# Kernel tuning notes

Hardware: AMD Instinct MI355X
Metric: run time of the kernel (lower is better)

## Reference

```python
import jax, jax.numpy as jnp
from jax import lax
import numpy as np

B, Q, C = 128, 200, 92  # batch, num_queries, num_classes (0 = no-object)


def hungarian(cost):
    """Exact Hungarian assignment (augmenting-path / JV potentials, e-maxx form).
    cost: [n, n]. Returns col_of_row: [n] int32, the column matched to each row.
    Uses 1-based columns/rows internally; index 0 is the sentinel."""
    n = cost.shape[0]
    INF = jnp.asarray(1e9, cost.dtype)

    def solve_row(i, carry):
        u, v, p = carry
        p = p.at[0].set(jnp.int32(i))
        minv = jnp.full(n + 1, INF, cost.dtype)
        way = jnp.zeros(n + 1, jnp.int32)
        used = jnp.zeros(n + 1, bool)
        state = (u, v, p, minv, way, used, jnp.int32(0))

        def cond(s):
            _u, _v, _p, _minv, _way, _used, j0 = s
            return _p[j0] != 0

        def body(s):
            u, v, p, minv, way, used, j0 = s
            used = used.at[j0].set(True)
            i0 = p[j0]
            cur = cost[i0 - 1, :] - u[i0] - v[1:]          # reduced costs of row i0
            cur = jnp.where(used[1:], INF, cur)
            upd = cur < minv[1:]
            minv = minv.at[1:].set(jnp.where(upd, cur, minv[1:]))
            way = way.at[1:].set(jnp.where(upd, j0, way[1:]))
            masked = jnp.where(used[1:], INF, minv[1:])
            j1 = jnp.argmin(masked).astype(jnp.int32) + 1
            delta = masked[j1 - 1]
            zero = jnp.asarray(0, cost.dtype)
            u = u.at[p].add(jnp.where(used, delta, zero))  # u[p[j]] += delta for used j (rows distinct)
            v = jnp.where(used, v - delta, v)
            minv = jnp.where(used, minv, minv - delta)
            return (u, v, p, minv, way, used, j1)

        u, v, p, minv, way, used, j0 = lax.while_loop(cond, body, state)

        def aug_body(s):  # flip matching along the alternating path
            p, j0 = s
            j1 = way[j0]
            return p.at[j0].set(p[j1]), j1

        p, _ = lax.while_loop(lambda s: s[1] != 0, aug_body, (p, j0))
        return (u, v, p)

    u0 = jnp.zeros(n + 1, cost.dtype)
    v0 = jnp.zeros(n + 1, cost.dtype)
    p0 = jnp.zeros(n + 1, jnp.int32)
    _, _, p = lax.fori_loop(1, n + 1, solve_row, (u0, v0, p0))
    # p[j] = row matched to column j (1-based); invert to col per row (0-based)
    col_of_row = jnp.zeros(n, jnp.int32).at[p[1:] - 1].set(jnp.arange(n, dtype=jnp.int32))
    return col_of_row


def cost_matrix(pred_cat, pred_bbox, tar_cat, tar_bbox):
    b, q, c = pred_cat.shape
    log_probs = jax.nn.log_softmax(pred_cat, axis=-1)                  # [B,Qp,C]
    idx = jnp.broadcast_to(tar_cat[:, None, :], (b, q, q))             # [B,Qp,Qt]
    ce = -jnp.take_along_axis(log_probs, idx, axis=2)                  # CE(pred_i, tgt_j)
    d = pred_bbox[:, :, None, :] - tar_bbox[:, None, :, :]             # [B,Qp,Qt,4]
    ad = jnp.abs(d)
    sl1 = jnp.where(ad < 1.0, 0.5 * d * d, ad - 0.5).sum(-1)           # SmoothL1 (beta=1)
    mask = (tar_cat != 0).astype(sl1.dtype)[:, None, :]                # bbox loss only for real objects
    return ce + sl1 * mask                                             # [B,Qp,Qt]


def setup_inputs() -> dict:
    key = jax.random.key(0)
    k1, k2, k3, k4 = jax.random.split(key, 4)
    pred_cat = jax.random.normal(k1, (B, Q, C), dtype=jnp.float32)
    pred_bbox = jax.random.uniform(k2, (B, Q, 4), dtype=jnp.float32)
    tar_cat = jax.random.randint(k3, (B, Q), 0, C, dtype=jnp.int32)
    tar_bbox = jax.random.uniform(k4, (B, Q, 4), dtype=jnp.float32)
    return {"pred_cat": pred_cat, "pred_bbox": pred_bbox, "tar_cat": tar_cat, "tar_bbox": tar_bbox}


def reference(pred_cat, pred_bbox, tar_cat, tar_bbox):
    cost = cost_matrix(pred_cat, pred_bbox, tar_cat, tar_bbox)         # [B,Q,Q]
    col = jax.vmap(hungarian)(lax.stop_gradient(cost))                 # assignment on detached cost
    out = jnp.take_along_axis(cost, col[:, :, None], axis=2)[..., 0]   # [B,Q] per-query matched loss
    return out
```

## Files before the change

kernel.cpp:

```cpp
#include <hip/hip_runtime.h>
#include <math.h>

#define BB 128
#define QQ 200
#define CC 92
#define CMPAD (QQ * QQ + 64)

__device__ __forceinline__ int rdlane_i(int x, int l) { return __builtin_amdgcn_readlane(x, l); }
__device__ __forceinline__ float rdlane_f(float x, int l) {
    return __uint_as_float((unsigned)__builtin_amdgcn_readlane((int)__float_as_uint(x), l));
}

__device__ __forceinline__ float wave_fmin_bcast(float x) {
    float y;
#define DPPSTEP(ctrl) \
    y = __uint_as_float((unsigned)__builtin_amdgcn_update_dpp( \
            (int)__float_as_uint(x), (int)__float_as_uint(x), ctrl, 0xf, 0xf, false)); \
    x = fminf(x, y);
    DPPSTEP(0x111) DPPSTEP(0x112) DPPSTEP(0x114) DPPSTEP(0x118)
    DPPSTEP(0x142) DPPSTEP(0x143)
#undef DPPSTEP
    return rdlane_f(x, 63);
}

__global__ __launch_bounds__(256) void hungarian_fused(const float* __restrict__ pc,
                                                       const float* __restrict__ pb,
                                                       const int*   __restrict__ tc,
                                                       const float* __restrict__ tb,
                                                       float* __restrict__ out) {
    const int b = blockIdx.x;
    const int tid = threadIdx.x;
    const int w = tid >> 6;
    const int t = tid & 63;

    __shared__ __align__(16) float cm[CMPAD];
    __shared__ float lse_s[QQ];

    const float INF = 1e9f;
    const int nval = (t < 8) ? 4 : 3;

    int   cls[4];
    float tbx[4][4];
#pragma unroll
    for (int k = 0; k < 4; ++k) {
        if (k < nval) {
            int jj = t + 64 * k;
            cls[k] = tc[b * QQ + jj];
            const float4 v4 = *reinterpret_cast<const float4*>(tb + ((size_t)(b * QQ + jj)) * 4);
            tbx[k][0] = v4.x; tbx[k][1] = v4.y; tbx[k][2] = v4.z; tbx[k][3] = v4.w;
        } else {
            cls[k] = 0;
            tbx[k][0] = tbx[k][1] = tbx[k][2] = tbx[k][3] = 0.f;
        }
    }

    if (tid < QQ) {
        const float* row = pc + ((size_t)(b * QQ + tid)) * CC;
        float m = -INFINITY;
        for (int c = 0; c < CC; ++c) m = fmaxf(m, row[c]);
        float s = 0.f;
        for (int c = 0; c < CC; ++c) s += expf(row[c] - m);
        lse_s[tid] = m + logf(s);
    }
    __syncthreads();

    for (int i = w; i < QQ; i += 4) {
        const float4 pb4 = *reinterpret_cast<const float4*>(pb + ((size_t)(b * QQ + i)) * 4);
        const float pbb[4] = {pb4.x, pb4.y, pb4.z, pb4.w};
        const float lsei = lse_s[i];
        const float* pcrow = pc + ((size_t)(b * QQ + i)) * CC;
#pragma unroll
        for (int k = 0; k < 4; ++k) {
            if (k < nval) {
                float ce = lsei - pcrow[cls[k]];
                float sl1 = 0.f;
#pragma unroll
                for (int d = 0; d < 4; ++d) {
                    float df = pbb[d] - tbx[k][d];
                    float ad = fabsf(df);
                    sl1 += (ad < 1.f) ? 0.5f * df * df : (ad - 0.5f);
                }
                float mask = (cls[k] != 0) ? 1.f : 0.f;
                cm[i * QQ + t + 64 * k] = ce + sl1 * mask;
            }
        }
    }
    __syncthreads();

    if (tid >= 64) return;

    float v[4]     = {0.f, 0.f, 0.f, 0.f};
    int   pslot[4] = {0, 0, 0, 0};
    unsigned pp    = 0u;
    float uslot[4] = {0.f, 0.f, 0.f, 0.f};
    float minv[4];
    int   waysl[4];
    int   usedm;
    float usent;

    for (int i = 1; i <= QQ; ++i) {
        minv[0] = minv[1] = minv[2] = minv[3] = INF;
        waysl[0] = waysl[1] = waysl[2] = waysl[3] = 0;
        usedm = 0;
        usent = 0.f;
        int j0 = 0;
        float u0 = 0.f;
        const float* crow = cm + (i - 1) * QQ;
        float c0 = crow[t];
        float c1 = crow[64 + t];
        float c2 = crow[128 + t];
        float c3 = crow[192 + t];

        for (;;) {
            if (j0 > 0) {
                int s = (j0 - 1) >> 6;
                if (((j0 - 1) & 63) == t) usedm |= 1 << s;
            }

            float kv0, kv1, kv2, kv3;
            {
                float cur;
                cur = c0 - u0 - v[0];
                if (!(usedm & 1) && cur < minv[0]) { minv[0] = cur; waysl[0] = j0; }
                kv0 = (usedm & 1) ? INF : minv[0];
                cur = c1 - u0 - v[1];
                if (!(usedm & 2) && cur < minv[1]) { minv[1] = cur; waysl[1] = j0; }
                kv1 = (usedm & 2) ? INF : minv[1];
                cur = c2 - u0 - v[2];
                if (!(usedm & 4) && cur < minv[2]) { minv[2] = cur; waysl[2] = j0; }
                kv2 = (usedm & 4) ? INF : minv[2];
                cur = c3 - u0 - v[3];
                if (!(usedm & 8) && t < 8 && cur < minv[3]) { minv[3] = cur; waysl[3] = j0; }
                kv3 = ((usedm & 8) || t >= 8) ? INF : minv[3];
            }

            float gmin = wave_fmin_bcast(fminf(fminf(kv0, kv1), fminf(kv2, kv3)));
            float delta = gmin;

            unsigned long long m0 = __ballot(kv0 == gmin);
            unsigned long long m1 = __ballot(kv1 == gmin);
            unsigned long long m2 = __ballot(kv2 == gmin);
            unsigned long long m3 = __ballot(kv3 == gmin);
            int j1;
            if (m0)      j1 = 1   + (int)__builtin_ctzll(m0);
            else if (m1) j1 = 65  + (int)__builtin_ctzll(m1);
            else if (m2) j1 = 129 + (int)__builtin_ctzll(m2);
            else         j1 = 193 + (int)__builtin_ctzll(m3);

            int kk = (j1 - 1) >> 6, ln = (j1 - 1) & 63;
            float us = (kk == 0) ? uslot[0] : (kk == 1) ? uslot[1]
                      : (kk == 2) ? uslot[2] : uslot[3];
            int pi = (int)(((unsigned)rdlane_i((int)pp, ln) >> (kk * 8)) & 255u);

            int nr = (pi > 0 ? pi : 1) - 1;
            const float* nrow = cm + nr * QQ;
            float n0 = nrow[t];
            float n1 = nrow[64 + t];
            float n2 = nrow[128 + t];
            float n3 = nrow[192 + t];

            float u0n = rdlane_f(us, ln);

#pragma unroll
            for (int k = 0; k < 4; ++k) {
                if (usedm & (1 << k)) {
                    v[k] -= delta;
                    uslot[k] += delta;
                } else if (k < nval) {
                    minv[k] -= delta;
                }
            }
            usent += delta;

            if (pi == 0) { j0 = j1; break; }
            j0 = j1; u0 = u0n;
            c0 = n0; c1 = n1; c2 = n2; c3 = n3;
        }

        {
            int jj = j0;
            while (jj != 0) {
                int jm = jj - 1, km = jm >> 6, lm = jm & 63;
                int ws = (km == 0) ? waysl[0] : (km == 1) ? waysl[1]
                        : (km == 2) ? waysl[2] : waysl[3];
                int jn = rdlane_i(ws, lm);
                int pnew; float unew;
                if (jn == 0) {
                    pnew = i;
                    unew = usent;
                } else {
                    int jm2 = jn - 1, kn = jm2 >> 6, ln2 = jm2 & 63;
                    int   ps2 = (kn == 0) ? pslot[0] : (kn == 1) ? pslot[1]
                               : (kn == 2) ? pslot[2] : pslot[3];
                    float us2 = (kn == 0) ? uslot[0] : (kn == 1) ? uslot[1]
                               : (kn == 2) ? uslot[2] : uslot[3];
                    pnew = rdlane_i(ps2, ln2);
                    unew = rdlane_f(us2, ln2);
                }
                if (lm == t) {
                    pslot[km] = pnew;
                    uslot[km] = unew;
                    int sh = km * 8;
                    pp = (pp & ~(255u << sh)) | ((unsigned)pnew << sh);
                }
                jj = jn;
            }
        }
    }

#pragma unroll
    for (int k = 0; k < 4; ++k) {
        if (k < nval) {
            int jc = 1 + t + 64 * k;
            int row = pslot[k] - 1;
            out[b * QQ + row] = cm[row * QQ + (jc - 1)];
        }
    }
}

extern "C" void kernel_launch(void* const* d_in, const int* in_sizes, int n_in,
                              void* d_out, int out_size, void* d_ws, size_t ws_size,
                              hipStream_t stream) {
    const float* pred_cat  = (const float*)d_in[0];
    const float* pred_bbox = (const float*)d_in[1];
    const int*   tar_cat   = (const int*)d_in[2];
    const float* tar_bbox  = (const float*)d_in[3];
    float* out = (float*)d_out;
    (void)d_ws; (void)ws_size;

    hungarian_fused<<<BB, 256, 0, stream>>>(pred_cat, pred_bbox, tar_cat, tar_bbox, out);
}
```

Before: 1.381 ms.

## Speculatively prefetch the cost row of the runner-up column in the Hungarian loop

```diff
diff --git a/kernel.cpp b/kernel.cpp
--- a/kernel.cpp
+++ b/kernel.cpp
@@ -110,6 +110,11 @@
         float c1 = crow[64 + t];
         float c2 = crow[128 + t];
         float c3 = crow[192 + t];
+
+        int   j2p = 0;
+        int   spi = 0;
+        float su0 = 0.f;
+        float s0 = 0.f, s1 = 0.f, s2 = 0.f, s3 = 0.f;
 
         for (;;) {
             if (j0 > 0) {
@@ -148,18 +153,26 @@
             else         j1 = 193 + (int)__builtin_ctzll(m3);
 
             int kk = (j1 - 1) >> 6, ln = (j1 - 1) & 63;
-            float us = (kk == 0) ? uslot[0] : (kk == 1) ? uslot[1]
-                      : (kk == 2) ? uslot[2] : uslot[3];
-            int pi = (int)(((unsigned)rdlane_i((int)pp, ln) >> (kk * 8)) & 255u);
-
-            int nr = (pi > 0 ? pi : 1) - 1;
-            const float* nrow = cm + nr * QQ;
-            float n0 = nrow[t];
-            float n1 = nrow[64 + t];
-            float n2 = nrow[128 + t];
-            float n3 = nrow[192 + t];
-
-            float u0n = rdlane_f(us, ln);
+
+            int pi;
+            float n0, n1, n2, n3, u0n;
+            bool hit = (j1 == j2p);
+            if (hit) {
+                pi = spi;
+                n0 = s0; n1 = s1; n2 = s2; n3 = s3;
+                u0n = su0;
+            } else {
+                float us = (kk == 0) ? uslot[0] : (kk == 1) ? uslot[1]
+                          : (kk == 2) ? uslot[2] : uslot[3];
+                pi = (int)(((unsigned)rdlane_i((int)pp, ln) >> (kk * 8)) & 255u);
+                int nr = (pi > 0 ? pi : 1) - 1;
+                const float* nrow = cm + nr * QQ;
+                n0 = nrow[t];
+                n1 = nrow[64 + t];
+                n2 = nrow[128 + t];
+                n3 = nrow[192 + t];
+                u0n = rdlane_f(us, ln);
+            }
 
 #pragma unroll
             for (int k = 0; k < 4; ++k) {
@@ -171,6 +184,37 @@
                 }
             }
             usent += delta;
+
+            {
+                float q0 = kv0, q1 = kv1, q2 = kv2, q3 = kv3;
+                bool me = (t == ln);
+                if (me & (kk == 0)) q0 = INF;
+                if (me & (kk == 1)) q1 = INF;
+                if (me & (kk == 2)) q2 = INF;
+                if (me & (kk == 3)) q3 = INF;
+                float g2 = wave_fmin_bcast(fminf(fminf(q0, q1), fminf(q2, q3)));
+                unsigned long long b0 = __ballot(q0 == g2);
+                unsigned long long b1 = __ballot(q1 == g2);
+                unsigned long long b2 = __ballot(q2 == g2);
+                unsigned long long b3 = __ballot(q3 == g2);
+                int j2;
+                if (b0)      j2 = 1   + (int)__builtin_ctzll(b0);
+                else if (b1) j2 = 65  + (int)__builtin_ctzll(b1);
+                else if (b2) j2 = 129 + (int)__builtin_ctzll(b2);
+                else         j2 = 193 + (int)__builtin_ctzll(b3);
+                int k2 = (j2 - 1) >> 6, l2 = (j2 - 1) & 63;
+                spi = (int)(((unsigned)rdlane_i((int)pp, l2) >> (k2 * 8)) & 255u);
+                int nr2 = (spi > 0 ? spi : 1) - 1;
+                const float* srow = cm + nr2 * QQ;
+                s0 = srow[t];
+                s1 = srow[64 + t];
+                s2 = srow[128 + t];
+                s3 = srow[192 + t];
+                float us2 = (k2 == 0) ? uslot[0] : (k2 == 1) ? uslot[1]
+                           : (k2 == 2) ? uslot[2] : uslot[3];
+                su0 = rdlane_f(us2, l2);
+                j2p = j2;
+            }
 
             if (pi == 0) { j0 = j1; break; }
             j0 = j1; u0 = u0n;
```

After: 2.119 ms. 1.53x slower.

## Overlap cost-matrix construction with Hungarian solve via per-row ready flags

Applied to the files above, without the earlier changes.

```diff
diff --git a/kernel.cpp b/kernel.cpp
--- a/kernel.cpp
+++ b/kernel.cpp
@@ -34,60 +34,77 @@
     const int t = tid & 63;
 
     __shared__ __align__(16) float cm[CMPAD];
-    __shared__ float lse_s[QQ];
+    __shared__ int rdy[QQ];
 
     const float INF = 1e9f;
     const int nval = (t < 8) ? 4 : 3;
 
-    int   cls[4];
-    float tbx[4][4];
-#pragma unroll
-    for (int k = 0; k < 4; ++k) {
-        if (k < nval) {
-            int jj = t + 64 * k;
-            cls[k] = tc[b * QQ + jj];
-            const float4 v4 = *reinterpret_cast<const float4*>(tb + ((size_t)(b * QQ + jj)) * 4);
-            tbx[k][0] = v4.x; tbx[k][1] = v4.y; tbx[k][2] = v4.z; tbx[k][3] = v4.w;
-        } else {
-            cls[k] = 0;
-            tbx[k][0] = tbx[k][1] = tbx[k][2] = tbx[k][3] = 0.f;
-        }
-    }
-
-    if (tid < QQ) {
-        const float* row = pc + ((size_t)(b * QQ + tid)) * CC;
-        float m = -INFINITY;
-        for (int c = 0; c < CC; ++c) m = fmaxf(m, row[c]);
-        float s = 0.f;
-        for (int c = 0; c < CC; ++c) s += expf(row[c] - m);
-        lse_s[tid] = m + logf(s);
-    }
+    if (tid < QQ) rdy[tid] = 0;
     __syncthreads();
 
-    for (int i = w; i < QQ; i += 4) {
-        const float4 pb4 = *reinterpret_cast<const float4*>(pb + ((size_t)(b * QQ + i)) * 4);
-        const float pbb[4] = {pb4.x, pb4.y, pb4.z, pb4.w};
-        const float lsei = lse_s[i];
-        const float* pcrow = pc + ((size_t)(b * QQ + i)) * CC;
+    if (w > 0) {
+        const int base  = (w - 1) * 67;
+        const int count = (w == 3) ? 66 : 67;
+
+        int   cls[4];
+        float tbx[4][4];
 #pragma unroll
         for (int k = 0; k < 4; ++k) {
             if (k < nval) {
-                float ce = lsei - pcrow[cls[k]];
-                float sl1 = 0.f;
-#pragma unroll
-                for (int d = 0; d < 4; ++d) {
-                    float df = pbb[d] - tbx[k][d];
-                    float ad = fabsf(df);
-                    sl1 += (ad < 1.f) ? 0.5f * df * df : (ad - 0.5f);
-                }
-                float mask = (cls[k] != 0) ? 1.f : 0.f;
-                cm[i * QQ + t + 64 * k] = ce + sl1 * mask;
-            }
-        }
+                int jj = t + 64 * k;
+                cls[k] = tc[b * QQ + jj];
+                const float4 v4 = *reinterpret_cast<const float4*>(tb + ((size_t)(b * QQ + jj)) * 4);
+                tbx[k][0] = v4.x; tbx[k][1] = v4.y; tbx[k][2] = v4.z; tbx[k][3] = v4.w;
+            } else {
+                cls[k] = 0;
+                tbx[k][0] = tbx[k][1] = tbx[k][2] = tbx[k][3] = 0.f;
+            }
+        }
+
+        auto lse_row = [&](int r) -> float {
+            const float* row = pc + ((size_t)(b * QQ + r)) * CC;
+            float m = -INFINITY;
+            for (int c = 0; c < CC; ++c) m = fmaxf(m, row[c]);
+            float s = 0.f;
+            for (int c = 0; c < CC; ++c) s += expf(row[c] - m);
+            return m + logf(s);
+        };
+
+        auto fill_row = [&](int i, float lsei) {
+            const float4 pb4 = *reinterpret_cast<const float4*>(pb + ((size_t)(b * QQ + i)) * 4);
+            const float pbb[4] = {pb4.x, pb4.y, pb4.z, pb4.w};
+            const float* pcrow = pc + ((size_t)(b * QQ + i)) * CC;
+#pragma unroll
+            for (int k = 0; k < 4; ++k) {
+                if (k < nval) {
+                    float ce = lsei - pcrow[cls[k]];
+                    float sl1 = 0.f;
+#pragma unroll
+                    for (int d = 0; d < 4; ++d) {
+                        float df = pbb[d] - tbx[k][d];
+                        float ad = fabsf(df);
+                        sl1 += (ad < 1.f) ? 0.5f * df * df : (ad - 0.5f);
+                    }
+                    float mask = (cls[k] != 0) ? 1.f : 0.f;
+                    cm[i * QQ + t + 64 * k] = ce + sl1 * mask;
+                }
+            }
+            asm volatile("s_waitcnt lgkmcnt(0)" ::: "memory");
+            if (t == 0) ((volatile int*)rdy)[i] = 1;
+        };
+
+        float lse_a = 0.f;
+        if (t < count) lse_a = lse_row(base + t);
+        const int n1 = (count < 64) ? count : 64;
+        for (int r = 0; r < n1; ++r) fill_row(base + r, rdlane_f(lse_a, r));
+
+        if (count > 64) {
+            float lse_b = 0.f;
+            if (64 + t < count) lse_b = lse_row(base + 64 + t);
+            for (int r = 64; r < count; ++r) fill_row(base + r, rdlane_f(lse_b, r - 64));
+        }
+        return;
     }
-    __syncthreads();
-
-    if (tid >= 64) return;
 
     float v[4]     = {0.f, 0.f, 0.f, 0.f};
     int   pslot[4] = {0, 0, 0, 0};
@@ -97,8 +114,20 @@
     int   waysl[4];
     int   usedm;
     float usent;
+    int   watermark = 0;
 
     for (int i = 1; i <= QQ; ++i) {
+        while (watermark < i) {
+            int idx = watermark + t;
+            int f = (idx < QQ) ? ((volatile int*)rdy)[idx] : 1;
+            unsigned long long rm = __ballot(f != 0);
+            unsigned long long nrm = ~rm;
+            int adv = nrm ? (int)__builtin_ctzll(nrm) : 64;
+            if (adv == 0) __builtin_amdgcn_s_sleep(8);
+            watermark += adv;
+        }
+        asm volatile("" ::: "memory");
+
         minv[0] = minv[1] = minv[2] = minv[3] = INF;
         waysl[0] = waysl[1] = waysl[2] = waysl[3] = 0;
         usedm = 0;
```

After: 1.410 ms. 2.1% more time.

## Overlap cost-matrix build with Hungarian solve using per-row LDS ready flags

Applied to the files above, without the earlier changes.

```diff
diff --git a/kernel.cpp b/kernel.cpp
--- a/kernel.cpp
+++ b/kernel.cpp
@@ -23,6 +23,108 @@
     return rdlane_f(x, 63);
 }
 
+
+#define PHASE_BODY(I)                                                          \
+    do {                                                                       \
+        minv[0] = minv[1] = minv[2] = minv[3] = INF;                           \
+        waysl[0] = waysl[1] = waysl[2] = waysl[3] = 0;                         \
+        usedm = 0;                                                             \
+        usent = 0.f;                                                           \
+        int j0 = 0;                                                            \
+        float u0 = 0.f;                                                        \
+        const float* crow = cm + ((I) - 1) * QQ;                               \
+        float c0 = crow[t];                                                    \
+        float c1 = crow[64 + t];                                               \
+        float c2 = crow[128 + t];                                              \
+        float c3 = crow[192 + t];                                              \
+        for (;;) {                                                             \
+            if (j0 > 0) {                                                      \
+                int s = (j0 - 1) >> 6;                                         \
+                if (((j0 - 1) & 63) == t) usedm |= 1 << s;                     \
+            }                                                                  \
+            float kv0, kv1, kv2, kv3;                                          \
+            {                                                                  \
+                float cur;                                                     \
+                cur = c0 - u0 - v[0];                                          \
+                if (!(usedm & 1) && cur < minv[0]) { minv[0] = cur; waysl[0] = j0; } \
+                kv0 = (usedm & 1) ? INF : minv[0];                             \
+                cur = c1 - u0 - v[1];                                          \
+                if (!(usedm & 2) && cur < minv[1]) { minv[1] = cur; waysl[1] = j0; } \
+                kv1 = (usedm & 2) ? INF : minv[1];                             \
+                cur = c2 - u0 - v[2];                                          \
+                if (!(usedm & 4) && cur < minv[2]) { minv[2] = cur; waysl[2] = j0; } \
+                kv2 = (usedm & 4) ? INF : minv[2];                             \
+                cur = c3 - u0 - v[3];                                          \
+                if (!(usedm & 8) && t < 8 && cur < minv[3]) { minv[3] = cur; waysl[3] = j0; } \
+                kv3 = ((usedm & 8) || t >= 8) ? INF : minv[3];                 \
+            }                                                                  \
+            float gmin = wave_fmin_bcast(fminf(fminf(kv0, kv1), fminf(kv2, kv3))); \
+            float delta = gmin;                                                \
+            unsigned long long m0 = __ballot(kv0 == gmin);                     \
+            unsigned long long m1 = __ballot(kv1 == gmin);                     \
+            unsigned long long m2 = __ballot(kv2 == gmin);                     \
+            unsigned long long m3 = __ballot(kv3 == gmin);                     \
+            int j1;                                                            \
+            if (m0)      j1 = 1   + (int)__builtin_ctzll(m0);                  \
+            else if (m1) j1 = 65  + (int)__builtin_ctzll(m1);                  \
+            else if (m2) j1 = 129 + (int)__builtin_ctzll(m2);                  \
+            else         j1 = 193 + (int)__builtin_ctzll(m3);                  \
+            int kk = (j1 - 1) >> 6, ln = (j1 - 1) & 63;                        \
+            float us = (kk == 0) ? uslot[0] : (kk == 1) ? uslot[1]             \
+                      : (kk == 2) ? uslot[2] : uslot[3];                       \
+            int pi = (int)(((unsigned)rdlane_i((int)pp, ln) >> (kk * 8)) & 255u); \
+            int nr = (pi > 0 ? pi : 1) - 1;                                    \
+            const float* nrow = cm + nr * QQ;                                  \
+            float n0 = nrow[t];                                                \
+            float n1 = nrow[64 + t];                                           \
+            float n2 = nrow[128 + t];                                          \
+            float n3 = nrow[192 + t];                                          \
+            float u0n = rdlane_f(us, ln);                                      \
+            _Pragma("unroll")                                                  \
+            for (int k = 0; k < 4; ++k) {                                      \
+                if (usedm & (1 << k)) {                                        \
+                    v[k] -= delta;                                             \
+                    uslot[k] += delta;                                         \
+                } else if (k < nval) {                                         \
+                    minv[k] -= delta;                                          \
+                }                                                              \
+            }                                                                  \
+            usent += delta;                                                    \
+            if (pi == 0) { j0 = j1; break; }                                   \
+            j0 = j1; u0 = u0n;                                                 \
+            c0 = n0; c1 = n1; c2 = n2; c3 = n3;                                \
+        }                                                                      \
+        {                                                                      \
+            int jj = j0;                                                       \
+            while (jj != 0) {                                                  \
+                int jm = jj - 1, km = jm >> 6, lm = jm & 63;                   \
+                int ws = (km == 0) ? waysl[0] : (km == 1) ? waysl[1]           \
+                        : (km == 2) ? waysl[2] : waysl[3];                     \
+                int jn = rdlane_i(ws, lm);                                     \
+                int pnew; float unew;                                          \
+                if (jn == 0) {                                                 \
+                    pnew = (I);                                                \
+                    unew = usent;                                              \
+                } else {                                                       \
+                    int jm2 = jn - 1, kn = jm2 >> 6, ln2 = jm2 & 63;           \
+                    int   ps2 = (kn == 0) ? pslot[0] : (kn == 1) ? pslot[1]    \
+                               : (kn == 2) ? pslot[2] : pslot[3];              \
+                    float us2 = (kn == 0) ? uslot[0] : (kn == 1) ? uslot[1]    \
+                               : (kn == 2) ? uslot[2] : uslot[3];              \
+                    pnew = rdlane_i(ps2, ln2);                                 \
+                    unew = rdlane_f(us2, ln2);                                 \
+                }                                                              \
+                if (lm == t) {                                                 \
+                    pslot[km] = pnew;                                          \
+                    uslot[km] = unew;                                          \
+                    int sh = km * 8;                                           \
+                    pp = (pp & ~(255u << sh)) | ((unsigned)pnew << sh);        \
+                }                                                              \
+                jj = jn;                                                       \
+            }                                                                  \
+        }                                                                      \
+    } while (0)
+
 __global__ __launch_bounds__(256) void hungarian_fused(const float* __restrict__ pc,
                                                        const float* __restrict__ pb,
                                                        const int*   __restrict__ tc,
@@ -35,59 +137,75 @@
 
     __shared__ __align__(16) float cm[CMPAD];
     __shared__ float lse_s[QQ];
+    __shared__ int rdy[QQ];
 
     const float INF = 1e9f;
     const int nval = (t < 8) ? 4 : 3;
 
-    int   cls[4];
-    float tbx[4][4];
-#pragma unroll
-    for (int k = 0; k < 4; ++k) {
-        if (k < nval) {
-            int jj = t + 64 * k;
-            cls[k] = tc[b * QQ + jj];
-            const float4 v4 = *reinterpret_cast<const float4*>(tb + ((size_t)(b * QQ + jj)) * 4);
-            tbx[k][0] = v4.x; tbx[k][1] = v4.y; tbx[k][2] = v4.z; tbx[k][3] = v4.w;
-        } else {
-            cls[k] = 0;
-            tbx[k][0] = tbx[k][1] = tbx[k][2] = tbx[k][3] = 0.f;
-        }
-    }
+    if (tid < QQ) rdy[tid] = 0;
 
     if (tid < QQ) {
-        const float* row = pc + ((size_t)(b * QQ + tid)) * CC;
+        const float4* row4 = reinterpret_cast<const float4*>(pc + ((size_t)(b * QQ + tid)) * CC);
         float m = -INFINITY;
-        for (int c = 0; c < CC; ++c) m = fmaxf(m, row[c]);
+        for (int c4 = 0; c4 < CC / 4; ++c4) {
+            float4 x = row4[c4];
+            m = fmaxf(fmaxf(fmaxf(fmaxf(m, x.x), x.y), x.z), x.w);
+        }
         float s = 0.f;
-        for (int c = 0; c < CC; ++c) s += expf(row[c] - m);
+        for (int c4 = 0; c4 < CC / 4; ++c4) {
+            float4 x = row4[c4];
+            s += expf(x.x - m); s += expf(x.y - m);
+            s += expf(x.z - m); s += expf(x.w - m);
+        }
         lse_s[tid] = m + logf(s);
     }
     __syncthreads();
 
-    for (int i = w; i < QQ; i += 4) {
-        const float4 pb4 = *reinterpret_cast<const float4*>(pb + ((size_t)(b * QQ + i)) * 4);
-        const float pbb[4] = {pb4.x, pb4.y, pb4.z, pb4.w};
-        const float lsei = lse_s[i];
-        const float* pcrow = pc + ((size_t)(b * QQ + i)) * CC;
+    if (w > 0) {
+        const int start = w - 1;
+        const int count = (QQ - start + 2) / 3;
+
+        int   cls[4];
+        float tbx[4][4];
 #pragma unroll
         for (int k = 0; k < 4; ++k) {
             if (k < nval) {
-                float ce = lsei - pcrow[cls[k]];
-                float sl1 = 0.f;
-#pragma unroll
-                for (int d = 0; d < 4; ++d) {
-                    float df = pbb[d] - tbx[k][d];
-                    float ad = fabsf(df);
-                    sl1 += (ad < 1.f) ? 0.5f * df * df : (ad - 0.5f);
+                int jj = t + 64 * k;
+                cls[k] = tc[b * QQ + jj];
+                const float4 v4 = *reinterpret_cast<const float4*>(tb + ((size_t)(b * QQ + jj)) * 4);
+                tbx[k][0] = v4.x; tbx[k][1] = v4.y; tbx[k][2] = v4.z; tbx[k][3] = v4.w;
+            } else {
+                cls[k] = 0;
+                tbx[k][0] = tbx[k][1] = tbx[k][2] = tbx[k][3] = 0.f;
+            }
+        }
+
+        for (int m = 0; m < count; ++m) {
+            const int i = start + 3 * m;
+            const float4 pb4 = *reinterpret_cast<const float4*>(pb + ((size_t)(b * QQ + i)) * 4);
+            const float pbb[4] = {pb4.x, pb4.y, pb4.z, pb4.w};
+            const float lsei = lse_s[i];
+            const float* pcrow = pc + ((size_t)(b * QQ + i)) * CC;
+#pragma unroll
+            for (int k = 0; k < 4; ++k) {
+                if (k < nval) {
+                    float ce = lsei - pcrow[cls[k]];
+                    float sl1 = 0.f;
+#pragma unroll
+                    for (int d = 0; d < 4; ++d) {
+                        float df = pbb[d] - tbx[k][d];
+                        float ad = fabsf(df);
+                        sl1 += (ad < 1.f) ? 0.5f * df * df : (ad - 0.5f);
+                    }
+                    float mask = (cls[k] != 0) ? 1.f : 0.f;
+                    cm[i * QQ + t + 64 * k] = ce + sl1 * mask;
                 }
-                float mask = (cls[k] != 0) ? 1.f : 0.f;
-                cm[i * QQ + t + 64 * k] = ce + sl1 * mask;
             }
-        }
-    }
-    __syncthreads();
-
-    if (tid >= 64) return;
+            asm volatile("s_waitcnt lgkmcnt(0)" ::: "memory");
+            if (t == 0) ((volatile int*)rdy)[i] = 1;
+        }
+        return;
+    }
 
     float v[4]     = {0.f, 0.f, 0.f, 0.f};
     int   pslot[4] = {0, 0, 0, 0};
@@ -97,115 +215,24 @@
     int   waysl[4];
     int   usedm;
     float usent;
-
-    for (int i = 1; i <= QQ; ++i) {
-        minv[0] = minv[1] = minv[2] = minv[3] = INF;
-        waysl[0] = waysl[1] = waysl[2] = waysl[3] = 0;
-        usedm = 0;
-        usent = 0.f;
-        int j0 = 0;
-        float u0 = 0.f;
-        const float* crow = cm + (i - 1) * QQ;
-        float c0 = crow[t];
-        float c1 = crow[64 + t];
-        float c2 = crow[128 + t];
-        float c3 = crow[192 + t];
-
-        for (;;) {
-            if (j0 > 0) {
-                int s = (j0 - 1) >> 6;
-                if (((j0 - 1) & 63) == t) usedm |= 1 << s;
-            }
-
-            float kv0, kv1, kv2, kv3;
-            {
-                float cur;
-                cur = c0 - u0 - v[0];
-                if (!(usedm & 1) && cur < minv[0]) { minv[0] = cur; waysl[0] = j0; }
-                kv0 = (usedm & 1) ? INF : minv[0];
-                cur = c1 - u0 - v[1];
-                if (!(usedm & 2) && cur < minv[1]) { minv[1] = cur; waysl[1] = j0; }
-                kv1 = (usedm & 2) ? INF : minv[1];
-                cur = c2 - u0 - v[2];
-                if (!(usedm & 4) && cur < minv[2]) { minv[2] = cur; waysl[2] = j0; }
-                kv2 = (usedm & 4) ? INF : minv[2];
-                cur = c3 - u0 - v[3];
-                if (!(usedm & 8) && t < 8 && cur < minv[3]) { minv[3] = cur; waysl[3] = j0; }
-                kv3 = ((usedm & 8) || t >= 8) ? INF : minv[3];
-            }
-
-            float gmin = wave_fmin_bcast(fminf(fminf(kv0, kv1), fminf(kv2, kv3)));
-            float delta = gmin;
-
-            unsigned long long m0 = __ballot(kv0 == gmin);
-            unsigned long long m1 = __ballot(kv1 == gmin);
-            unsigned long long m2 = __ballot(kv2 == gmin);
-            unsigned long long m3 = __ballot(kv3 == gmin);
-            int j1;
-            if (m0)      j1 = 1   + (int)__builtin_ctzll(m0);
-            else if (m1) j1 = 65  + (int)__builtin_ctzll(m1);
-            else if (m2) j1 = 129 + (int)__builtin_ctzll(m2);
-            else         j1 = 193 + (int)__builtin_ctzll(m3);
-
-            int kk = (j1 - 1) >> 6, ln = (j1 - 1) & 63;
-            float us = (kk == 0) ? uslot[0] : (kk == 1) ? uslot[1]
-                      : (kk == 2) ? uslot[2] : uslot[3];
-            int pi = (int)(((unsigned)rdlane_i((int)pp, ln) >> (kk * 8)) & 255u);
-
-            int nr = (pi > 0 ? pi : 1) - 1;
-            const float* nrow = cm + nr * QQ;
-            float n0 = nrow[t];
-            float n1 = nrow[64 + t];
-            float n2 = nrow[128 + t];
-            float n3 = nrow[192 + t];
-
-            float u0n = rdlane_f(us, ln);
-
-#pragma unroll
-            for (int k = 0; k < 4; ++k) {
-                if (usedm & (1 << k)) {
-                    v[k] -= delta;
-                    uslot[k] += delta;
-                } else if (k < nval) {
-                    minv[k] -= delta;
-                }
-            }
-            usent += delta;
-
-            if (pi == 0) { j0 = j1; break; }
-            j0 = j1; u0 = u0n;
-            c0 = n0; c1 = n1; c2 = n2; c3 = n3;
-        }
-
-        {
-            int jj = j0;
-            while (jj != 0) {
-                int jm = jj - 1, km = jm >> 6, lm = jm & 63;
-                int ws = (km == 0) ? waysl[0] : (km == 1) ? waysl[1]
-                        : (km == 2) ? waysl[2] : waysl[3];
-                int jn = rdlane_i(ws, lm);
-                int pnew; float unew;
-                if (jn == 0) {
-                    pnew = i;
-                    unew = usent;
-                } else {
-                    int jm2 = jn - 1, kn = jm2 >> 6, ln2 = jm2 & 63;
-                    int   ps2 = (kn == 0) ? pslot[0] : (kn == 1) ? pslot[1]
-                               : (kn == 2) ? pslot[2] : pslot[3];
-                    float us2 = (kn == 0) ? uslot[0] : (kn == 1) ? uslot[1]
-                               : (kn == 2) ? uslot[2] : uslot[3];
-                    pnew = rdlane_i(ps2, ln2);
-                    unew = rdlane_f(us2, ln2);
-                }
-                if (lm == t) {
-                    pslot[km] = pnew;
-                    uslot[km] = unew;
-                    int sh = km * 8;
-                    pp = (pp & ~(255u << sh)) | ((unsigned)pnew << sh);
-                }
-                jj = jn;
-            }
-        }
+    int   watermark = 0;
+    int   i = 1;
+
+    for (; i <= QQ && watermark < QQ; ++i) {
+        while (watermark < i) {
+            int idx = watermark + t;
+            int f = (idx < QQ) ? ((volatile int*)rdy)[idx] : 1;
+            unsigned long long rm = __ballot(f != 0);
+            unsigned long long nrm = ~rm;
+            int adv = nrm ? (int)__builtin_ctzll(nrm) : 64;
+            if (adv == 0) __builtin_amdgcn_s_sleep(8);
+            watermark += adv;
+        }
+        asm volatile("" ::: "memory");
+        PHASE_BODY(i);
+    }
+    for (; i <= QQ; ++i) {
+        PHASE_BODY(i);
     }
 
 #pragma unroll
```

After: 1.368 ms, median of 2. About the same (-1.0%).
